# Kernel tuning notes

Hardware: AMD Instinct MI355X
Metric: run time of the kernel (lower is better)

## Reference

```python
import jax, jax.numpy as jnp
import numpy as np

BATCH, SEQ, HIDDEN, HEADS = 2, 2048, 2048, 16
HEAD_DIM = HIDDEN // HEADS
NEG_INF = -1e9


def setup_inputs() -> dict:
    key = jax.random.key(0)
    ks = jax.random.split(key, 5)
    scale = 1.0 / np.sqrt(HIDDEN)
    hidden_states = jax.random.normal(ks[0], (BATCH, SEQ, HIDDEN), dtype=jnp.float32)
    q_proj = jax.random.normal(ks[1], (HIDDEN, HIDDEN), dtype=jnp.float32) * scale
    k_proj = jax.random.normal(ks[2], (HIDDEN, HIDDEN), dtype=jnp.float32) * scale
    v_proj = jax.random.normal(ks[3], (HIDDEN, HIDDEN), dtype=jnp.float32) * scale
    o_proj = jax.random.normal(ks[4], (HIDDEN, HIDDEN), dtype=jnp.float32) * scale
    # additive causal mask [B, 1, S, S]: 0 on/below diagonal, -1e9 above
    causal = jnp.tril(jnp.ones((SEQ, SEQ), dtype=bool))
    attention_mask = jnp.where(causal, 0.0, NEG_INF).astype(jnp.float32)[None, None, :, :]
    attention_mask = jnp.broadcast_to(attention_mask, (BATCH, 1, SEQ, SEQ))
    return {
        "hidden_states": hidden_states,
        "attention_mask": attention_mask,
        "q_proj": q_proj,
        "k_proj": k_proj,
        "v_proj": v_proj,
        "o_proj": o_proj,
    }


def reference(hidden_states, attention_mask, q_proj, k_proj, v_proj, o_proj):
    B, S, _ = hidden_states.shape
    # QKV projections, split into heads: [B, H, S, D]
    q = (hidden_states @ q_proj).reshape(B, S, HEADS, HEAD_DIM).transpose(0, 2, 1, 3)
    k = (hidden_states @ k_proj).reshape(B, S, HEADS, HEAD_DIM).transpose(0, 2, 1, 3)
    v = (hidden_states @ v_proj).reshape(B, S, HEADS, HEAD_DIM).transpose(0, 2, 1, 3)
    # scores [B, H, S, S]
    scores = jnp.einsum("bhqd,bhkd->bhqk", q, k) / jnp.sqrt(jnp.float32(HEAD_DIM))
    scores = scores + attention_mask
    probs = jax.nn.softmax(scores, axis=-1)
    context = jnp.einsum("bhqk,bhkd->bhqd", probs, v)
    context = context.transpose(0, 2, 1, 3).reshape(B, S, HIDDEN)
    return context @ o_proj
```

## Files before the change

### kernel.cpp

```cpp
#include <hip/hip_runtime.h>

#define SEQ      2048
#define HIDDEN   2048
#define HEADS    16
#define HEAD_DIM 128
#define NTOK     4096
#define WSZ      4194304

typedef short s16x8 __attribute__((ext_vector_type(8)));
typedef float f32x4 __attribute__((ext_vector_type(4)));
typedef unsigned short ushort_t;
typedef unsigned int u32;
typedef u32 __attribute__((address_space(1))) gu32;
typedef u32 __attribute__((address_space(3))) lu32;

__device__ __forceinline__ unsigned short f2bf(float f) {
    union { float f; unsigned int u; } c; c.f = f;
    unsigned int r = (c.u + 0x7FFFu + ((c.u >> 16) & 1u)) >> 16;
    return (unsigned short)r;
}
__device__ __forceinline__ float bf2f(unsigned short h) {
    union { unsigned int u; float f; } c; c.u = ((unsigned int)h) << 16;
    return c.f;
}
__device__ __forceinline__ f32x4 mfma16(s16x8 a, s16x8 b, f32x4 c) {
    return __builtin_amdgcn_mfma_f32_16x16x32_bf16(a, b, c, 0, 0, 0);
}
__device__ __forceinline__ void async_copy16(const void* g, void* l) {
    __builtin_amdgcn_global_load_lds((const gu32*)g, (lu32*)l, 16, 0, 0);
}

__global__ __launch_bounds__(256) void convert_hs_kernel(const float* __restrict__ hs,
                                                         ushort_t* __restrict__ Ah,
                                                         ushort_t* __restrict__ Al)
{
    size_t i = ((size_t)blockIdx.x * 256 + threadIdx.x) * 4;
    float4 v = *(const float4*)&hs[i];
    ushort4 hi, lo;
    hi.x = f2bf(v.x); lo.x = f2bf(v.x - bf2f(hi.x));
    hi.y = f2bf(v.y); lo.y = f2bf(v.y - bf2f(hi.y));
    hi.z = f2bf(v.z); lo.z = f2bf(v.z - bf2f(hi.z));
    hi.w = f2bf(v.w); lo.w = f2bf(v.w - bf2f(hi.w));
    *(ushort4*)&Ah[i] = hi;
    *(ushort4*)&Al[i] = lo;
}

__global__ __launch_bounds__(256) void convert_w_kernel(const float* __restrict__ Wa,
                                                        const float* __restrict__ Wb,
                                                        const float* __restrict__ Wc,
                                                        ushort_t* __restrict__ dst)
{
    __shared__ float t[32][33];
    const int z = blockIdx.z;
    const float* W = (z == 0) ? Wa : (z == 1) ? Wb : Wc;
    ushort_t* oh = dst + (size_t)z * 2 * WSZ;
    ushort_t* ol = oh + WSZ;
    const int tx = threadIdx.x & 31, ty = threadIdx.x >> 5;
    const int k0 = blockIdx.y << 5, n0 = blockIdx.x << 5;
#pragma unroll
    for (int r = 0; r < 4; r++)
        t[ty + r * 8][tx] = W[(size_t)(k0 + ty + r * 8) * HIDDEN + n0 + tx];
    __syncthreads();
#pragma unroll
    for (int r = 0; r < 4; r++) {
        int n = n0 + ty + r * 8;
        float x = t[tx][ty + r * 8];
        ushort_t hb = f2bf(x);
        oh[(size_t)n * HIDDEN + k0 + tx] = hb;
        ol[(size_t)n * HIDDEN + k0 + tx] = f2bf(x - bf2f(hb));
    }
}

__device__ __forceinline__ void mfma_gemm_body(const ushort_t* __restrict__ Ah,
                                               const ushort_t* __restrict__ Al,
                                               const ushort_t* __restrict__ BhT,
                                               const ushort_t* __restrict__ BlT,
                                               int mode, float oscale,
                                               void* __restrict__ out0,
                                               void* __restrict__ out1)
{
    __shared__ ushort_t lds[4][4096];
    const int tid  = threadIdx.x;
    const int w    = tid >> 6, lane = tid & 63;
    const int lq   = lane & 15, g16 = lane >> 4;
    const int wr   = w >> 1, wc = w & 1;
    const int row0 = blockIdx.y << 7;
    const int col0 = blockIdx.x << 7;

    const ushort_t* a_h = Ah  + (size_t)row0 * HIDDEN;
    const ushort_t* a_l = Al  + (size_t)row0 * HIDDEN;
    const ushort_t* b_h = BhT + (size_t)col0 * HIDDEN;
    const ushort_t* b_l = BlT + (size_t)col0 * HIDDEN;

    f32x4 acc[4][4] = {};

    for (int kt = 0; kt < HIDDEN; kt += 32) {
        __syncthreads();
#pragma unroll
        for (int u = 0; u < 2; u++) {
            const int phys = w * 2048 + u * 1024 + lane * 16;
            const int prow = phys >> 6;
            const int pke  = (((phys & 63) ^ ((prow & 3) << 4)) >> 1);
            const size_t go = (size_t)prow * HIDDEN + kt + pke;
            const int lofs = w * 1024 + u * 512;
            async_copy16(a_h + go, &lds[0][lofs]);
            async_copy16(a_l + go, &lds[1][lofs]);
            async_copy16(b_h + go, &lds[2][lofs]);
            async_copy16(b_l + go, &lds[3][lofs]);
        }
        __syncthreads();

        s16x8 ah[4], al[4], bh[4], bl[4];
#pragma unroll
        for (int i = 0; i < 4; i++) {
            int r  = wr * 64 + i * 16 + lq;
            int pb = r * 64 + ((g16 * 16) ^ ((r & 3) << 4));
            ah[i] = *(const s16x8*)((const char*)&lds[0][0] + pb);
            al[i] = *(const s16x8*)((const char*)&lds[1][0] + pb);
        }
#pragma unroll
        for (int j = 0; j < 4; j++) {
            int r  = wc * 64 + j * 16 + lq;
            int pb = r * 64 + ((g16 * 16) ^ ((r & 3) << 4));
            bh[j] = *(const s16x8*)((const char*)&lds[2][0] + pb);
            bl[j] = *(const s16x8*)((const char*)&lds[3][0] + pb);
        }
#pragma unroll
        for (int i = 0; i < 4; i++)
#pragma unroll
            for (int j = 0; j < 4; j++) {
                acc[i][j] = mfma16(ah[i], bh[j], acc[i][j]);
                acc[i][j] = mfma16(ah[i], bl[j], acc[i][j]);
                acc[i][j] = mfma16(al[i], bh[j], acc[i][j]);
            }
    }

#pragma unroll
    for (int i = 0; i < 4; i++) {
        const int rbase = row0 + wr * 64 + i * 16 + g16 * 4;
#pragma unroll
        for (int j = 0; j < 4; j++) {
            const int col = col0 + wc * 64 + j * 16 + lq;
            if (mode == 0) {
                float* o = (float*)out0;
#pragma unroll
                for (int r = 0; r < 4; r++)
                    o[(size_t)(rbase + r) * HIDDEN + col] = acc[i][j][r];
            } else if (mode == 1) {
                const int h = col >> 7, d = col & 127;
#pragma unroll
                for (int r = 0; r < 4; r++) {
                    int rowg = rbase + r;
                    int bb = rowg >> 11, s = rowg & 2047;
                    size_t idx = ((size_t)(bb * HEADS + h) * SEQ + s) * HEAD_DIM + d;
                    float x = acc[i][j][r] * oscale;
                    ushort_t hb = f2bf(x);
                    ((ushort_t*)out0)[idx] = hb;
                    ((ushort_t*)out1)[idx] = f2bf(x - bf2f(hb));
                }
            } else {
                const int h = col >> 7, d = col & 127;
                const int bb = rbase >> 11, s0 = rbase & 2047;
                ushort4 pv;
                pv.x = f2bf(acc[i][j][0]); pv.y = f2bf(acc[i][j][1]);
                pv.z = f2bf(acc[i][j][2]); pv.w = f2bf(acc[i][j][3]);
                *(ushort4*)&((ushort_t*)out0)[((size_t)(bb * HEADS + h) * HEAD_DIM + d) * SEQ + s0] = pv;
            }
        }
    }
}

__global__ __launch_bounds__(256) void qkv_gemm_mfma(const ushort_t* __restrict__ Ah,
                                                     const ushort_t* __restrict__ Al,
                                                     const ushort_t* __restrict__ wT,
                                                     ushort_t* qhi, ushort_t* qlo,
                                                     ushort_t* khi, ushort_t* klo,
                                                     ushort_t* vt)
{
    const int z = blockIdx.z;
    const ushort_t* BhT = wT + (size_t)z * 2 * WSZ;
    const ushort_t* BlT = BhT + WSZ;
    int   mode = (z == 2) ? 2 : 1;
    float osc  = (z == 0) ? 0.08838834764831845f : 1.0f;
    void* o0 = (z == 0) ? (void*)qhi : (z == 1) ? (void*)khi : (void*)vt;
    void* o1 = (z == 0) ? (void*)qlo : (z == 1) ? (void*)klo : nullptr;
    mfma_gemm_body(Ah, Al, BhT, BlT, mode, osc, o0, o1);
}

__global__ __launch_bounds__(256) void o_gemm_mfma(const ushort_t* __restrict__ Ah,
                                                   const ushort_t* __restrict__ Al,
                                                   const ushort_t* __restrict__ wT,
                                                   float* __restrict__ out)
{
    mfma_gemm_body(Ah, Al, wT, wT + WSZ, 0, 1.0f, out, nullptr);
}

__global__ __launch_bounds__(256) void attn_kernel(const ushort_t* __restrict__ qhi_g,
                                                   const ushort_t* __restrict__ qlo_g,
                                                   const ushort_t* __restrict__ khi_g,
                                                   const ushort_t* __restrict__ klo_g,
                                                   const ushort_t* __restrict__ vt_g,
                                                   ushort_t* __restrict__ ctxh,
                                                   ushort_t* __restrict__ ctxl)
{
    __shared__ ushort_t Kh[64][136];
    __shared__ ushort_t Kl[64][136];
    __shared__ ushort_t Vtile[128][72];
    __shared__ ushort_t Ps[4][16][72];

    const int tid  = threadIdx.x;
    const int w    = tid >> 6;
    const int lane = tid & 63;
    const int lq   = lane & 15;
    const int g    = lane >> 4;
    const int head = blockIdx.y;
    const int bb   = head >> 4, h = head & 15;

    const ushort_t* kh_head = khi_g + (size_t)head * SEQ * HEAD_DIM;
    const ushort_t* kl_head = klo_g + (size_t)head * SEQ * HEAD_DIM;
    const ushort_t* vt_head = vt_g  + (size_t)head * HEAD_DIM * SEQ;

#pragma unroll 1
    for (int half = 0; half < 2; half++) {
        const int qb = half ? (31 - blockIdx.x) : blockIdx.x;
        const int r0 = qb << 6;
        const int nkt = qb + 1;

        s16x8 qh[4], ql[4];
        {
            const size_t qbase = ((size_t)head * SEQ + r0 + w * 16 + lq) * HEAD_DIM;
#pragma unroll
            for (int dblk = 0; dblk < 4; dblk++) {
                qh[dblk] = *(const s16x8*)(&qhi_g[qbase + dblk * 32 + 8 * g]);
                ql[dblk] = *(const s16x8*)(&qlo_g[qbase + dblk * 32 + 8 * g]);
            }
        }

        float m_run = -1e30f, l_run = 0.f;
        f32x4 acc[8] = {};

#pragma unroll 1
        for (int kt = 0; kt < nkt; kt++) {
            __syncthreads();
            {
                const ushort_t* khs = kh_head + (size_t)(kt * 64) * HEAD_DIM;
                const ushort_t* kls = kl_head + (size_t)(kt * 64) * HEAD_DIM;
#pragma unroll
                for (int u = 0; u < 4; u++) {
                    int idx = tid + u * 256;
                    int kr = idx >> 4, c16 = idx & 15;
                    *(int4*)(&Kh[kr][c16 * 8]) =
                        *(const int4*)(&khs[(size_t)kr * HEAD_DIM + c16 * 8]);
                    *(int4*)(&Kl[kr][c16 * 8]) =
                        *(const int4*)(&kls[(size_t)kr * HEAD_DIM + c16 * 8]);
                }
                const ushort_t* vs = vt_head + kt * 64;
#pragma unroll
                for (int u = 0; u < 4; u++) {
                    int idx = tid + u * 256;
                    int vr = idx >> 3, c8 = idx & 7;
                    *(int4*)(&Vtile[vr][c8 * 8]) =
                        *(const int4*)(&vs[(size_t)vr * SEQ + c8 * 8]);
                }
            }
            __syncthreads();

            f32x4 sc[4] = {};
#pragma unroll
            for (int dblk = 0; dblk < 4; dblk++) {
#pragma unroll
                for (int kb = 0; kb < 4; kb++) {
                    const int rowb = kb * 16 + lq;
                    s16x8 ahf = *(const s16x8*)(&Kh[rowb][dblk * 32 + 8 * g]);
                    s16x8 alf = *(const s16x8*)(&Kl[rowb][dblk * 32 + 8 * g]);
                    sc[kb] = mfma16(ahf, qh[dblk], sc[kb]);
                    sc[kb] = mfma16(alf, qh[dblk], sc[kb]);
                    sc[kb] = mfma16(ahf, ql[dblk], sc[kb]);
                }
            }

            if (kt == nkt - 1) {
                const int qloc = w * 16 + lq;
#pragma unroll
                for (int kb = 0; kb < 4; kb++)
#pragma unroll
                    for (int r = 0; r < 4; r++)
                        if (kb * 16 + 4 * g + r > qloc) sc[kb][r] = -1e30f;
            }

            float mx = -1e30f;
#pragma unroll
            for (int kb = 0; kb < 4; kb++)
#pragma unroll
                for (int r = 0; r < 4; r++) mx = fmaxf(mx, sc[kb][r]);
            mx = fmaxf(mx, __shfl_xor(mx, 16));
            mx = fmaxf(mx, __shfl_xor(mx, 32));
            float mnew = fmaxf(m_run, mx);
            float fs = __expf(m_run - mnew);
            float sum = 0.f;
            f32x4 p[4];
#pragma unroll
            for (int kb = 0; kb < 4; kb++)
#pragma unroll
                for (int r = 0; r < 4; r++) {
                    float e = __expf(sc[kb][r] - mnew);
                    p[kb][r] = e;
                    sum += e;
                }
            sum += __shfl_xor(sum, 16);
            sum += __shfl_xor(sum, 32);
            l_run = l_run * fs + sum;
            m_run = mnew;
#pragma unroll
            for (int d = 0; d < 8; d++) acc[d] *= fs;

#pragma unroll
            for (int kb = 0; kb < 4; kb++) {
                ushort4 pw;
                pw.x = f2bf(p[kb][0]); pw.y = f2bf(p[kb][1]);
                pw.z = f2bf(p[kb][2]); pw.w = f2bf(p[kb][3]);
                *(ushort4*)(&Ps[w][lq][kb * 16 + 4 * g]) = pw;
            }
            __builtin_amdgcn_s_waitcnt(0);
            __builtin_amdgcn_sched_barrier(0);

#pragma unroll
            for (int k0 = 0; k0 < 2; k0++) {
                s16x8 pb = *(const s16x8*)(&Ps[w][lq][k0 * 32 + 8 * g]);
#pragma unroll
                for (int dblk = 0; dblk < 8; dblk++) {
                    s16x8 av = *(const s16x8*)(&Vtile[dblk * 16 + lq][k0 * 32 + 8 * g]);
                    acc[dblk] = mfma16(av, pb, acc[dblk]);
                }
            }
        }

        {
            float inv = 1.f / l_run;
            int sg = r0 + w * 16 + lq;
            size_t obase = ((size_t)bb * SEQ + sg) * HIDDEN + h * HEAD_DIM + 4 * g;
#pragma unroll
            for (int dblk = 0; dblk < 8; dblk++) {
                ushort4 hv, lv;
                float x0 = acc[dblk][0] * inv, x1 = acc[dblk][1] * inv;
                float x2 = acc[dblk][2] * inv, x3 = acc[dblk][3] * inv;
                hv.x = f2bf(x0); lv.x = f2bf(x0 - bf2f(hv.x));
                hv.y = f2bf(x1); lv.y = f2bf(x1 - bf2f(hv.y));
                hv.z = f2bf(x2); lv.z = f2bf(x2 - bf2f(hv.z));
                hv.w = f2bf(x3); lv.w = f2bf(x3 - bf2f(hv.w));
                *(ushort4*)&ctxh[obase + dblk * 16] = hv;
                *(ushort4*)&ctxl[obase + dblk * 16] = lv;
            }
        }
    }
}

extern "C" void kernel_launch(void* const* d_in, const int* in_sizes, int n_in,
                              void* d_out, int out_size, void* d_ws, size_t ws_size,
                              hipStream_t stream)
{
    (void)in_sizes; (void)n_in; (void)out_size; (void)ws_size;
    const float* hs = (const float*)d_in[0];
    const float* wq = (const float*)d_in[2];
    const float* wk = (const float*)d_in[3];
    const float* wv = (const float*)d_in[4];
    const float* wo = (const float*)d_in[5];
    float* out = (float*)d_out;

    const size_t NH = (size_t)NTOK * HIDDEN;
    ushort_t* wT  = (ushort_t*)d_ws;
    ushort_t* Ah  = wT + 6 * (size_t)WSZ;
    ushort_t* Al  = Ah + NH;
    ushort_t* qhi = Al + NH;
    ushort_t* qlo = qhi + NH;
    ushort_t* khi = qlo + NH;
    ushort_t* klo = khi + NH;
    ushort_t* vt  = klo + NH;
    ushort_t* ctxh = Ah;
    ushort_t* ctxl = Al;
    ushort_t* woT  = wT;

    convert_hs_kernel<<<NH / 1024, 256, 0, stream>>>(hs, Ah, Al);
    convert_w_kernel<<<dim3(64, 64, 3), 256, 0, stream>>>(wq, wk, wv, wT);

    qkv_gemm_mfma<<<dim3(HIDDEN / 128, NTOK / 128, 3), 256, 0, stream>>>(
        Ah, Al, wT, qhi, qlo, khi, klo, vt);

    attn_kernel<<<dim3(16, 2 * HEADS), 256, 0, stream>>>(
        qhi, qlo, khi, klo, vt, ctxh, ctxl);

    convert_w_kernel<<<dim3(64, 64, 1), 256, 0, stream>>>(wo, wo, wo, woT);

    o_gemm_mfma<<<dim3(HIDDEN / 128, NTOK / 128, 1), 256, 0, stream>>>(
        ctxh, ctxl, woT, out);
}
```

Measured before the change: 693.2 us.

## Interleave hi/lo tiles in LDS and remap GEMM blocks XCD-aware

Changes the GEMM LDS layout so that each row holds the hi and lo bf16 halves side by side in a 128-byte row with an 8-way XOR swizzle. Each thread now issues one 16-byte async copy per matrix per row group instead of separate hi/lo copies. The GEMM grids are flattened to 1D and remapped so that consecutive blocks on the same XCD (flat&7) work on contiguous tiles, which should improve L2 reuse across the MI355X's chiplets. The added risk is the more complex index math and possible LDS bank conflicts from the new swizzle.

```diff
diff --git a/kernel.cpp b/kernel.cpp
--- a/kernel.cpp
+++ b/kernel.cpp
@@ -75,38 +75,35 @@
                                                const ushort_t* __restrict__ Al,
                                                const ushort_t* __restrict__ BhT,
                                                const ushort_t* __restrict__ BlT,
+                                               int row0, int col0,
                                                int mode, float oscale,
                                                void* __restrict__ out0,
                                                void* __restrict__ out1)
 {
-    __shared__ ushort_t lds[4][4096];
+    __shared__ ushort_t lds[2][128][64];
     const int tid  = threadIdx.x;
     const int w    = tid >> 6, lane = tid & 63;
     const int lq   = lane & 15, g16 = lane >> 4;
     const int wr   = w >> 1, wc = w & 1;
-    const int row0 = blockIdx.y << 7;
-    const int col0 = blockIdx.x << 7;
-
-    const ushort_t* a_h = Ah  + (size_t)row0 * HIDDEN;
-    const ushort_t* a_l = Al  + (size_t)row0 * HIDDEN;
-    const ushort_t* b_h = BhT + (size_t)col0 * HIDDEN;
-    const ushort_t* b_l = BlT + (size_t)col0 * HIDDEN;
+
+    const int  trow  = tid >> 3;
+    const int  lcol  = ((tid & 7) << 4) ^ ((trow & 7) << 4);
+    const int  kelem = (lcol & 63) >> 1;
+    const bool lo    = (lcol & 64) != 0;
+    const ushort_t* srcA = (lo ? Al : Ah) + (size_t)(row0 + trow) * HIDDEN + kelem;
+    const ushort_t* srcB = (lo ? BlT : BhT) + (size_t)(col0 + trow) * HIDDEN + kelem;
+    char* ldsA = (char*)&lds[0][0][0];
+    char* ldsB = (char*)&lds[1][0][0];
+    const int dstoff = tid * 16;
 
     f32x4 acc[4][4] = {};
 
     for (int kt = 0; kt < HIDDEN; kt += 32) {
         __syncthreads();
 #pragma unroll
-        for (int u = 0; u < 2; u++) {
-            const int phys = w * 2048 + u * 1024 + lane * 16;
-            const int prow = phys >> 6;
-            const int pke  = (((phys & 63) ^ ((prow & 3) << 4)) >> 1);
-            const size_t go = (size_t)prow * HIDDEN + kt + pke;
-            const int lofs = w * 1024 + u * 512;
-            async_copy16(a_h + go, &lds[0][lofs]);
-            async_copy16(a_l + go, &lds[1][lofs]);
-            async_copy16(b_h + go, &lds[2][lofs]);
-            async_copy16(b_l + go, &lds[3][lofs]);
+        for (int u = 0; u < 4; u++) {
+            async_copy16(srcA + kt + (size_t)u * 32 * HIDDEN, ldsA + dstoff + u * 4096);
+            async_copy16(srcB + kt + (size_t)u * 32 * HIDDEN, ldsB + dstoff + u * 4096);
         }
         __syncthreads();
 
@@ -114,16 +111,16 @@
 #pragma unroll
         for (int i = 0; i < 4; i++) {
             int r  = wr * 64 + i * 16 + lq;
-            int pb = r * 64 + ((g16 * 16) ^ ((r & 3) << 4));
-            ah[i] = *(const s16x8*)((const char*)&lds[0][0] + pb);
-            al[i] = *(const s16x8*)((const char*)&lds[1][0] + pb);
+            int ph = r * 128 + ((g16 * 16) ^ ((r & 7) << 4));
+            ah[i] = *(const s16x8*)(ldsA + ph);
+            al[i] = *(const s16x8*)(ldsA + (ph ^ 64));
         }
 #pragma unroll
         for (int j = 0; j < 4; j++) {
             int r  = wc * 64 + j * 16 + lq;
-            int pb = r * 64 + ((g16 * 16) ^ ((r & 3) << 4));
-            bh[j] = *(const s16x8*)((const char*)&lds[2][0] + pb);
-            bl[j] = *(const s16x8*)((const char*)&lds[3][0] + pb);
+            int ph = r * 128 + ((g16 * 16) ^ ((r & 7) << 4));
+            bh[j] = *(const s16x8*)(ldsB + ph);
+            bl[j] = *(const s16x8*)(ldsB + (ph ^ 64));
         }
 #pragma unroll
         for (int i = 0; i < 4; i++)
@@ -177,14 +174,20 @@
                                                      ushort_t* khi, ushort_t* klo,
                                                      ushort_t* vt)
 {
-    const int z = blockIdx.z;
+    const int flat = blockIdx.x;
+    const int nf   = (flat & 7) * 192 + (flat >> 3);
+    const int z    = nf >> 9;
+    const int rem  = nf & 511;
+    const int row0 = (rem >> 4) << 7;
+    const int col0 = (rem & 15) << 7;
+
     const ushort_t* BhT = wT + (size_t)z * 2 * WSZ;
     const ushort_t* BlT = BhT + WSZ;
     int   mode = (z == 2) ? 2 : 1;
     float osc  = (z == 0) ? 0.08838834764831845f : 1.0f;
     void* o0 = (z == 0) ? (void*)qhi : (z == 1) ? (void*)khi : (void*)vt;
     void* o1 = (z == 0) ? (void*)qlo : (z == 1) ? (void*)klo : nullptr;
-    mfma_gemm_body(Ah, Al, BhT, BlT, mode, osc, o0, o1);
+    mfma_gemm_body(Ah, Al, BhT, BlT, row0, col0, mode, osc, o0, o1);
 }
 
 __global__ __launch_bounds__(256) void o_gemm_mfma(const ushort_t* __restrict__ Ah,
@@ -192,7 +195,11 @@
                                                    const ushort_t* __restrict__ wT,
                                                    float* __restrict__ out)
 {
-    mfma_gemm_body(Ah, Al, wT, wT + WSZ, 0, 1.0f, out, nullptr);
+    const int flat = blockIdx.x;
+    const int nf   = (flat & 7) * 64 + (flat >> 3);
+    const int row0 = (nf >> 4) << 7;
+    const int col0 = (nf & 15) << 7;
+    mfma_gemm_body(Ah, Al, wT, wT + WSZ, row0, col0, 0, 1.0f, out, nullptr);
 }
 
 __global__ __launch_bounds__(256) void attn_kernel(const ushort_t* __restrict__ qhi_g,
@@ -383,14 +390,12 @@
     convert_hs_kernel<<<NH / 1024, 256, 0, stream>>>(hs, Ah, Al);
     convert_w_kernel<<<dim3(64, 64, 3), 256, 0, stream>>>(wq, wk, wv, wT);
 
-    qkv_gemm_mfma<<<dim3(HIDDEN / 128, NTOK / 128, 3), 256, 0, stream>>>(
-        Ah, Al, wT, qhi, qlo, khi, klo, vt);
+    qkv_gemm_mfma<<<1536, 256, 0, stream>>>(Ah, Al, wT, qhi, qlo, khi, klo, vt);
 
     attn_kernel<<<dim3(16, 2 * HEADS), 256, 0, stream>>>(
         qhi, qlo, khi, klo, vt, ctxh, ctxl);
 
     convert_w_kernel<<<dim3(64, 64, 1), 256, 0, stream>>>(wo, wo, wo, woT);
 
-    o_gemm_mfma<<<dim3(HIDDEN / 128, NTOK / 128, 1), 256, 0, stream>>>(
-        ctxh, ctxl, woT, out);
-}
+    o_gemm_mfma<<<512, 256, 0, stream>>>(ctxh, ctxl, woT, out);
+}
```

Result: no change. 703.4 us (+1.5%).
